# Optimization experiments

Hardware: AMD Instinct MI355X
Metric: run time of the kernel (lower is better)

The kernel has to match this reference:

```python
import jax, jax.numpy as jnp
import numpy as np

B, S, E, H, V, L = 128, 64, 300, 512, 100000, 5


def _linear_params(k, din, dout):
    k1, k2 = jax.random.split(k)
    w = jax.random.normal(k1, (dout, din), jnp.float32) * (1.0 / np.sqrt(din))
    b = jax.random.normal(k2, (dout,), jnp.float32) * 0.01
    return w, b


def setup_inputs() -> dict:
    key = jax.random.key(0)
    ks = jax.random.split(key, 12)
    inp = {}
    inp["x"] = jax.random.randint(ks[0], (B, S), 0, V)              # word ids
    inp["bfs"] = jax.random.randint(ks[1], (B, S), 0, S)            # processing order (node index per step)
    inp["children"] = jax.random.randint(ks[2], (B, S, S), 0, 2).astype(jnp.int32)  # binary child adjacency
    inp["embed"] = jax.random.normal(ks[3], (V, E), jnp.float32) * 0.1
    names = ["ix", "ih", "fx", "fh", "ux", "uh"]
    dims = [(E, H), (H, H), (E, H), (H, H), (E, H), (H, H)]
    for n, (di, do), k in zip(names, dims, ks[4:10]):
        w, b = _linear_params(k, di, do)
        inp["W" + n] = w
        inp["b" + n] = b
    w, b = _linear_params(ks[10], H, L)
    inp["Wout"] = w
    inp["bout"] = b
    return inp


def reference(x, bfs, children, embed,
              Wix, bix, Wih, bih, Wfx, bfx, Wfh, bfh, Wux, bux, Wuh, buh,
              Wout, bout):
    # Child-Sum TreeLSTM processed in BFS order. Dropouts are eval-mode (identity).
    Bb, Ss = x.shape
    Hh = Wih.shape[0]
    xe_all = embed[x]                     # [B,S,E]
    pos = jnp.arange(Ss)

    def step(carry, cur):
        all_C, all_H, _ = carry           # all_C/all_H: [B,S,H]; cur: [B] node index this step
        xe = jnp.take_along_axis(xe_all, cur[:, None, None], axis=1)[:, 0]            # [B,E]
        cmask = jnp.take_along_axis(children, cur[:, None, None], axis=1)[:, 0]       # [B,S]
        cmask = cmask.astype(xe.dtype)
        h_sum = jnp.einsum('bs,bsh->bh', cmask, all_H)                                # sum of child hiddens
        fx_x = xe @ Wfx.T + bfx
        i = jax.nn.sigmoid(xe @ Wix.T + bix + h_sum @ Wih.T + bih)
        # NOTE: faithful to source — the 'o' gate uses fx/fh (ox/oh are dead params)
        o = jax.nn.sigmoid(fx_x + h_sum @ Wfh.T + bfh)
        u = jnp.tanh(xe @ Wux.T + bux + h_sum @ Wuh.T + buh)
        f = jax.nn.sigmoid(all_H @ Wfh.T + bfh + fx_x[:, None, :])                    # [B,S,H] per-child forget
        fc = jnp.einsum('bs,bsh->bh', cmask, f * all_C)                               # masked sum over children
        c = i * u + fc                                                                 # [B,H]
        h = o * jnp.tanh(c)
        onehot = (pos[None, :] == cur[:, None])[:, :, None]                           # [B,S,1]
        all_C = jnp.where(onehot, c[:, None, :], all_C)
        all_H = jnp.where(onehot, h[:, None, :], all_H)
        return (all_C, all_H, h), None

    init = (jnp.zeros((Bb, Ss, Hh), embed.dtype),
            jnp.zeros((Bb, Ss, Hh), embed.dtype),
            jnp.zeros((Bb, Hh), embed.dtype))
    (_, _, h_last), _ = jax.lax.scan(step, init, bfs.T)  # scan over sent_len steps
    return h_last @ Wout.T + bout                        # [B, label_num]
```

## Files before the change

### kernel.cpp

```cpp
#include <hip/hip_runtime.h>
#include <math.h>

#define BB 128
#define SS 64
#define EE 300
#define HH 512
#define LL 5
#define BSH (BB*SS*HH)
#define KP  320
#define NGRP 8
#define BPG  32
#define HSL  16
#define WSROW 520
#define HS_BASE (2*3*16*WSROW)
#define WS_BYTES ((2*3*16*WSROW + 2*16*WSROW)*2)

typedef __attribute__((ext_vector_type(8))) short bf16x8;
typedef __attribute__((ext_vector_type(4))) float f32x4;
typedef __attribute__((ext_vector_type(4))) unsigned int u32x4;

__device__ __forceinline__ float fast_sigmoid(float x) {
    return 1.0f / (1.0f + __expf(-x));
}
__device__ __forceinline__ float fast_tanh(float x) {
    x = fminf(fmaxf(x, -20.0f), 20.0f);
    float e = __expf(2.0f * x);
    return (e - 1.0f) / (e + 1.0f);
}
__device__ __forceinline__ unsigned short f2bf(float f) {
    unsigned int u = __float_as_uint(f);
    u += 0x7fffu + ((u >> 16) & 1u);
    return (unsigned short)(u >> 16);
}
__device__ __forceinline__ float bf2f(unsigned short h) {
    return __uint_as_float((unsigned int)h << 16);
}
__device__ __forceinline__ void split2(float v, unsigned short& hi, unsigned short& lo) {
    hi = f2bf(v);
    lo = f2bf(v - bf2f(hi));
}

#define LDX4V(dst, addr) \
    asm volatile("global_load_dwordx4 %0, %1, off sc0 sc1" \
                 : "=v"(dst) : "v"(addr))

#define STH(addr, val) \
    asm volatile("global_store_short %0, %1, off sc0 sc1" \
                 :: "v"(addr), "v"(val) : "memory")

__global__ __launch_bounds__(256) void prep_kernel(
    const int* __restrict__ bfs, const int* __restrict__ children,
    const float* __restrict__ Wix, const float* __restrict__ Wfx, const float* __restrict__ Wux,
    const float* __restrict__ Wih, const float* __restrict__ Wfh, const float* __restrict__ Wuh,
    unsigned short* __restrict__ Wixh, unsigned short* __restrict__ Wixl,
    unsigned short* __restrict__ Wfxh, unsigned short* __restrict__ Wfxl,
    unsigned short* __restrict__ Wuxh, unsigned short* __restrict__ Wuxl,
    unsigned short* __restrict__ Wihh, unsigned short* __restrict__ Wihl,
    unsigned short* __restrict__ Wfhh, unsigned short* __restrict__ Wfhl,
    unsigned short* __restrict__ Wuhh, unsigned short* __restrict__ Wuhl,
    unsigned char* __restrict__ clist, int* __restrict__ ccnt, int* __restrict__ bars)
{
    const int gid = blockIdx.x * 256 + threadIdx.x;
    const int G = gridDim.x * 256;
    for (int i = gid; i < NGRP * SS; i += G) bars[i] = 0;
    for (int i = gid; i < 3 * HH * KP; i += G) {
        int g = i / (HH * KP), rem = i % (HH * KP), r = rem / KP, k = rem % KP;
        const float* src = (g == 0) ? Wix : (g == 1) ? Wfx : Wux;
        unsigned short* dh = (g == 0) ? Wixh : (g == 1) ? Wfxh : Wuxh;
        unsigned short* dl = (g == 0) ? Wixl : (g == 1) ? Wfxl : Wuxl;
        float v = (k < EE) ? src[(size_t)r * EE + k] : 0.0f;
        unsigned short hi, lo; split2(v, hi, lo);
        dh[r * KP + k] = hi; dl[r * KP + k] = lo;
    }
    for (int i = gid; i < 3 * HH * HH; i += G) {
        int g = i / (HH * HH), idx = i % (HH * HH);
        const float* src = (g == 0) ? Wih : (g == 1) ? Wfh : Wuh;
        unsigned short* dh = (g == 0) ? Wihh : (g == 1) ? Wfhh : Wuhh;
        unsigned short* dl = (g == 0) ? Wihl : (g == 1) ? Wfhl : Wuhl;
        unsigned short hi, lo; split2(src[idx], hi, lo);
        dh[idx] = hi; dl[idx] = lo;
    }
    if (gid < BB * SS) {
        const int b = gid >> 6, t = gid & 63;
        unsigned long long w = 0;
        for (int tp = 0; tp < t; ++tp) w |= 1ull << (bfs[b * SS + tp] & 63);
        const int cur = bfs[b * SS + t];
        const int* crow = children + (size_t)(b * SS + cur) * SS;
        unsigned char* lst = clist + (size_t)gid * SS;
        int cnt = 0;
        for (int s = 0; s < SS; ++s)
            if (crow[s] != 0 && ((w >> s) & 1ull)) lst[cnt++] = (unsigned char)s;
        ccnt[gid] = cnt;
    }
}

__global__ __launch_bounds__(256) void xp_mfma(
    const int* __restrict__ x, const float* __restrict__ embed,
    const unsigned short* __restrict__ Wixh, const unsigned short* __restrict__ Wixl,
    const unsigned short* __restrict__ Wfxh, const unsigned short* __restrict__ Wfxl,
    const unsigned short* __restrict__ Wuxh, const unsigned short* __restrict__ Wuxl,
    const float* __restrict__ bix, const float* __restrict__ bih,
    const float* __restrict__ bfx, const float* __restrict__ bfh,
    const float* __restrict__ bux, const float* __restrict__ buh,
    float* __restrict__ XPp)
{
    const int mb = blockIdx.x;
    const int g  = blockIdx.y;
    const unsigned short* __restrict__ Wbh = (g == 0) ? Wixh : (g == 1) ? Wfxh : Wuxh;
    const unsigned short* __restrict__ Wbl = (g == 0) ? Wixl : (g == 1) ? Wfxl : Wuxl;
    const float* __restrict__ b1 = (g == 0) ? bix : (g == 1) ? bfx : bux;
    const float* __restrict__ b2 = (g == 0) ? bih : (g == 1) ? bfh : buh;

    const int row0 = mb * 16;
    __shared__ unsigned short As[2][16 * 328];
    __shared__ int toks[16];

    const int tid = threadIdx.x;
    if (tid < 16) toks[tid] = x[row0 + tid];
    __syncthreads();

    for (int i = tid; i < 16 * 75; i += 256) {
        int r = i / 75, c = i - r * 75;
        const float4 v = *(const float4*)(embed + (size_t)toks[r] * EE + c * 4);
        ushort4 hv, lv;
        split2(v.x, hv.x, lv.x); split2(v.y, hv.y, lv.y);
        split2(v.z, hv.z, lv.z); split2(v.w, hv.w, lv.w);
        *(ushort4*)&As[0][r * 328 + c * 4] = hv;
        *(ushort4*)&As[1][r * 328 + c * 4] = lv;
    }
    for (int i = tid; i < 16 * 20; i += 256) {
        int r = i / 20, k = EE + (i - r * 20);
        As[0][r * 328 + k] = 0; As[1][r * 328 + k] = 0;
    }
    __syncthreads();

    const int lane = tid & 63, wave = tid >> 6;
    const int quad = lane >> 4, col = lane & 15;
    const int wn = wave * 16;

    for (int nt = 0; nt < 8; ++nt) {
        const int gn = nt * 64 + wn + col;
        const size_t wrow = (size_t)gn * KP;
        f32x4 accA = {0.f, 0.f, 0.f, 0.f}, accB = {0.f, 0.f, 0.f, 0.f};
        #pragma unroll
        for (int kq = 0; kq < 10; ++kq) {
            const int ka = kq * 32 + quad * 8;
            bf16x8 bh = *(const bf16x8*)(Wbh + wrow + ka);
            bf16x8 bl = *(const bf16x8*)(Wbl + wrow + ka);
            bf16x8 ah = *(const bf16x8*)&As[0][col * 328 + ka];
            bf16x8 al = *(const bf16x8*)&As[1][col * 328 + ka];
            accA = __builtin_amdgcn_mfma_f32_16x16x32_bf16(ah, bh, accA, 0, 0, 0);
            accB = __builtin_amdgcn_mfma_f32_16x16x32_bf16(ah, bl, accB, 0, 0, 0);
            accA = __builtin_amdgcn_mfma_f32_16x16x32_bf16(al, bh, accA, 0, 0, 0);
        }
        const f32x4 acc = accA + accB;
        const float bb = b1[gn] + b2[gn];
        #pragma unroll
        for (int reg = 0; reg < 4; ++reg) {
            const int ml = quad * 4 + reg;
            XPp[((size_t)(row0 + ml) * HH + gn) * 4 + g] = acc[reg] + bb;
        }
    }
}

__global__ __launch_bounds__(256, 1) void fused_steps(
    const int* __restrict__ bfs, const unsigned char* __restrict__ clist,
    const int* __restrict__ ccnt, const float* __restrict__ XPp,
    const unsigned short* __restrict__ Wihh, const unsigned short* __restrict__ Wihl,
    const unsigned short* __restrict__ Wfhh, const unsigned short* __restrict__ Wfhl,
    const unsigned short* __restrict__ Wuhh, const unsigned short* __restrict__ Wuhl,
    float* __restrict__ HWC, float* __restrict__ hf32,
    unsigned short* __restrict__ h_hi, unsigned short* __restrict__ h_lo,
    int* __restrict__ bars)
{
    extern __shared__ unsigned short Ws[];
    __shared__ int s_cur[16 * 64];
    __shared__ int s_cnt[16 * 64];
    __shared__ unsigned char s_cl[16 * 64];

    const int g = blockIdx.x & 7;
    const int l = blockIdx.x >> 3;
    const int tid = threadIdx.x;
    const int m0 = g * 16;
    const int n0 = l * HSL;

    const int lane = tid & 63, wave = tid >> 6;
    const int quad = lane >> 4, col = lane & 15;

    const int chain = tid >> 4, hl = tid & 15;
    const int b = m0 + chain;
    const int h = n0 + hl;

    {
        for (int i = tid; i < 6144; i += 256) {
            const int plane = i / 3072, rem = i % 3072;
            const int gt = rem / 1024, rem2 = rem % 1024;
            const int r = rem2 >> 6, c = rem2 & 63;
            const unsigned short* src =
                (plane == 0) ? ((gt == 0) ? Wihh : (gt == 1) ? Wfhh : Wuhh)
                             : ((gt == 0) ? Wihl : (gt == 1) ? Wfhl : Wuhl);
            *(u32x4*)&Ws[((plane * 3 + gt) * 16 + r) * WSROW + c * 8] =
                *(const u32x4*)(src + (size_t)(n0 + r) * HH + c * 8);
        }
        for (int i = tid; i < 16 * 64; i += 256) {
            s_cur[i] = bfs[(m0 + (i >> 6)) * SS + (i & 63)];
            s_cnt[i] = ccnt[(m0 + (i >> 6)) * SS + (i & 63)];
        }
        if (tid < 64) {
            const int ch = tid >> 2, c = tid & 3;
            ((u32x4*)s_cl)[tid] =
                *(const u32x4*)(clist + ((size_t)(m0 + ch) * SS + 0) * SS + c * 16);
        }
    }
    __syncthreads();

    const size_t browf = (size_t)b * (SS * HH * 4);
    float4 xp_c, xp_n;
    {
        const int cur0 = s_cur[(chain << 6) + 0];
        xp_c = *(const float4*)(XPp + browf + (size_t)cur0 * (HH * 4) + h * 4);
    }

    int* gbars = bars + g * SS;

    int st_p[8], st_ch[8], st_o16[8];
    #pragma unroll
    for (int j = 0; j < 8; ++j) {
        const int i = j * 256 + tid;
        st_p[j] = i >> 10; st_ch[j] = (i & 1023) >> 6; st_o16[j] = i & 63;
    }

    for (int t = 0; t < SS; ++t) {
        const int cur = s_cur[(chain << 6) + t];
        const int cnt = s_cnt[(chain << 6) + t];
        const float xpi = xp_c.x, xpf = xp_c.y, xpu = xp_c.z;
        const float* HWb = HWC + browf + h * 4;
        const unsigned char* clp = &s_cl[chain << 6];

        float ai = 0.f, af = 0.f, au = 0.f, fc = 0.f;
        int idx = 0;
        while (idx + 8 <= cnt) {
            const float4 v0 = *(const float4*)(HWb + (size_t)clp[idx + 0] * 2048);
            const float4 v1 = *(const float4*)(HWb + (size_t)clp[idx + 1] * 2048);
            const float4 v2 = *(const float4*)(HWb + (size_t)clp[idx + 2] * 2048);
            const float4 v3 = *(const float4*)(HWb + (size_t)clp[idx + 3] * 2048);
            const float4 v4 = *(const float4*)(HWb + (size_t)clp[idx + 4] * 2048);
            const float4 v5 = *(const float4*)(HWb + (size_t)clp[idx + 5] * 2048);
            const float4 v6 = *(const float4*)(HWb + (size_t)clp[idx + 6] * 2048);
            const float4 v7 = *(const float4*)(HWb + (size_t)clp[idx + 7] * 2048);
            ai += v0.x + v1.x + v2.x + v3.x + v4.x + v5.x + v6.x + v7.x;
            af += v0.y + v1.y + v2.y + v3.y + v4.y + v5.y + v6.y + v7.y;
            au += v0.z + v1.z + v2.z + v3.z + v4.z + v5.z + v6.z + v7.z;
            fc += fast_sigmoid(v0.y + xpf) * v0.w + fast_sigmoid(v1.y + xpf) * v1.w
                + fast_sigmoid(v2.y + xpf) * v2.w + fast_sigmoid(v3.y + xpf) * v3.w
                + fast_sigmoid(v4.y + xpf) * v4.w + fast_sigmoid(v5.y + xpf) * v5.w
                + fast_sigmoid(v6.y + xpf) * v6.w + fast_sigmoid(v7.y + xpf) * v7.w;
            idx += 8;
        }
        while (idx + 4 <= cnt) {
            const float4 v0 = *(const float4*)(HWb + (size_t)clp[idx + 0] * 2048);
            const float4 v1 = *(const float4*)(HWb + (size_t)clp[idx + 1] * 2048);
            const float4 v2 = *(const float4*)(HWb + (size_t)clp[idx + 2] * 2048);
            const float4 v3 = *(const float4*)(HWb + (size_t)clp[idx + 3] * 2048);
            ai += v0.x + v1.x + v2.x + v3.x;
            af += v0.y + v1.y + v2.y + v3.y;
            au += v0.z + v1.z + v2.z + v3.z;
            fc += fast_sigmoid(v0.y + xpf) * v0.w + fast_sigmoid(v1.y + xpf) * v1.w
                + fast_sigmoid(v2.y + xpf) * v2.w + fast_sigmoid(v3.y + xpf) * v3.w;
            idx += 4;
        }
        while (idx < cnt) {
            const float4 v = *(const float4*)(HWb + (size_t)clp[idx] * 2048);
            ai += v.x; af += v.y; au += v.z;
            fc += fast_sigmoid(v.y + xpf) * v.w;
            ++idx;
        }

        const float ig = fast_sigmoid(xpi + ai);
        const float og = fast_sigmoid(xpf + af);
        const float ug = fast_tanh(xpu + au);
        const float c  = ig * ug + fc;
        const float hv = og * fast_tanh(c);

        HWC[browf + (size_t)cur * 2048 + h * 4 + 3] = c;
        if (t == SS - 1) {
            hf32[(size_t)b * HH + h] = hv;
            break;
        }
        {
            unsigned short hh_s, hlo_s; split2(hv, hh_s, hlo_s);
            const unsigned long long ah = (unsigned long long)(h_hi + (size_t)b * HH + h);
            const unsigned long long al = (unsigned long long)(h_lo + (size_t)b * HH + h);
            STH(ah, (unsigned int)hh_s);
            STH(al, (unsigned int)hlo_s);
        }

        __asm__ volatile("s_waitcnt vmcnt(0)" ::: "memory");
        __syncthreads();

        {
            const int curn = s_cur[(chain << 6) + t + 1];
            xp_n = *(const float4*)(XPp + browf + (size_t)curn * (HH * 4) + h * 4);
        }
        if (tid == 0) {
            int* cntp = gbars + t;
            __hip_atomic_fetch_add(cntp, 1, __ATOMIC_RELAXED, __HIP_MEMORY_SCOPE_AGENT);
            while (__hip_atomic_load(cntp, __ATOMIC_RELAXED, __HIP_MEMORY_SCOPE_AGENT) < BPG)
                __builtin_amdgcn_s_sleep(1);
        }
        __syncthreads();

        if (wave == 3 && lane < 64) {
            const int ch = lane >> 2, cc = lane & 3;
            ((u32x4*)s_cl)[lane] =
                *(const u32x4*)(clist + ((size_t)(m0 + ch) * SS + (t + 1)) * SS + cc * 16);
        }
        {
            u32x4 st0, st1, st2, st3, st4, st5, st6, st7;
            const unsigned long long a0 = (unsigned long long)((st_p[0] ? h_lo : h_hi) + (size_t)(m0 + st_ch[0]) * HH + st_o16[0] * 8);
            const unsigned long long a1 = (unsigned long long)((st_p[1] ? h_lo : h_hi) + (size_t)(m0 + st_ch[1]) * HH + st_o16[1] * 8);
            const unsigned long long a2 = (unsigned long long)((st_p[2] ? h_lo : h_hi) + (size_t)(m0 + st_ch[2]) * HH + st_o16[2] * 8);
            const unsigned long long a3 = (unsigned long long)((st_p[3] ? h_lo : h_hi) + (size_t)(m0 + st_ch[3]) * HH + st_o16[3] * 8);
            const unsigned long long a4 = (unsigned long long)((st_p[4] ? h_lo : h_hi) + (size_t)(m0 + st_ch[4]) * HH + st_o16[4] * 8);
            const unsigned long long a5 = (unsigned long long)((st_p[5] ? h_lo : h_hi) + (size_t)(m0 + st_ch[5]) * HH + st_o16[5] * 8);
            const unsigned long long a6 = (unsigned long long)((st_p[6] ? h_lo : h_hi) + (size_t)(m0 + st_ch[6]) * HH + st_o16[6] * 8);
            const unsigned long long a7 = (unsigned long long)((st_p[7] ? h_lo : h_hi) + (size_t)(m0 + st_ch[7]) * HH + st_o16[7] * 8);
            LDX4V(st0, a0); LDX4V(st1, a1); LDX4V(st2, a2); LDX4V(st3, a3);
            LDX4V(st4, a4); LDX4V(st5, a5); LDX4V(st6, a6); LDX4V(st7, a7);
            asm volatile("s_waitcnt vmcnt(0)" ::: "memory");
            __builtin_amdgcn_sched_barrier(0);
            *(u32x4*)&Ws[HS_BASE + (st_p[0] * 16 + st_ch[0]) * WSROW + st_o16[0] * 8] = st0;
            *(u32x4*)&Ws[HS_BASE + (st_p[1] * 16 + st_ch[1]) * WSROW + st_o16[1] * 8] = st1;
            *(u32x4*)&Ws[HS_BASE + (st_p[2] * 16 + st_ch[2]) * WSROW + st_o16[2] * 8] = st2;
            *(u32x4*)&Ws[HS_BASE + (st_p[3] * 16 + st_ch[3]) * WSROW + st_o16[3] * 8] = st3;
            *(u32x4*)&Ws[HS_BASE + (st_p[4] * 16 + st_ch[4]) * WSROW + st_o16[4] * 8] = st4;
            *(u32x4*)&Ws[HS_BASE + (st_p[5] * 16 + st_ch[5]) * WSROW + st_o16[5] * 8] = st5;
            *(u32x4*)&Ws[HS_BASE + (st_p[6] * 16 + st_ch[6]) * WSROW + st_o16[6] * 8] = st6;
            *(u32x4*)&Ws[HS_BASE + (st_p[7] * 16 + st_ch[7]) * WSROW + st_o16[7] * 8] = st7;
        }
        __syncthreads();

        if (wave < 3) {
            f32x4 accA = {0.f, 0.f, 0.f, 0.f}, accB = {0.f, 0.f, 0.f, 0.f};
            const int ha0 = HS_BASE + (0 * 16 + col) * WSROW;
            const int ha1 = HS_BASE + (1 * 16 + col) * WSROW;
            #pragma unroll
            for (int kq = 0; kq < 16; ++kq) {
                const int ka = kq * 32 + quad * 8;
                bf16x8 ahv = *(const bf16x8*)&Ws[ha0 + ka];
                bf16x8 alv = *(const bf16x8*)&Ws[ha1 + ka];
                bf16x8 bh = *(const bf16x8*)&Ws[((0 * 3 + wave) * 16 + col) * WSROW + ka];
                bf16x8 bl = *(const bf16x8*)&Ws[((1 * 3 + wave) * 16 + col) * WSROW + ka];
                accA = __builtin_amdgcn_mfma_f32_16x16x32_bf16(ahv, bh, accA, 0, 0, 0);
                accB = __builtin_amdgcn_mfma_f32_16x16x32_bf16(ahv, bl, accB, 0, 0, 0);
                accA = __builtin_amdgcn_mfma_f32_16x16x32_bf16(alv, bh, accA, 0, 0, 0);
            }
            const f32x4 acc = accA + accB;
            #pragma unroll
            for (int reg = 0; reg < 4; ++reg) {
                const int m = quad * 4 + reg;
                const int curm = s_cur[(m << 6) + t];
                HWC[(size_t)(m0 + m) * (SS * HH * 4) + (size_t)curm * 2048
                    + (n0 + col) * 4 + wave] = acc[reg];
            }
        }
        __threadfence_block();
        __syncthreads();
        xp_c = xp_n;
    }
}

__global__ __launch_bounds__(64) void out_kernel(
    const float* __restrict__ hcur,
    const float* __restrict__ Wout, const float* __restrict__ bout,
    float* __restrict__ out)
{
    const int b = blockIdx.x;
    const int lane = threadIdx.x;
    float acc[LL];
    #pragma unroll
    for (int l = 0; l < LL; ++l) acc[l] = 0.0f;
    for (int h = lane; h < HH; h += 64) {
        const float hv = hcur[(size_t)b * HH + h];
        #pragma unroll
        for (int l = 0; l < LL; ++l) acc[l] += hv * Wout[l * HH + h];
    }
    #pragma unroll
    for (int off = 32; off > 0; off >>= 1) {
        #pragma unroll
        for (int l = 0; l < LL; ++l) acc[l] += __shfl_down(acc[l], off);
    }
    if (lane == 0) {
        #pragma unroll
        for (int l = 0; l < LL; ++l) out[b * LL + l] = acc[l] + bout[l];
    }
}

extern "C" void kernel_launch(void* const* d_in, const int* in_sizes, int n_in,
                              void* d_out, int out_size, void* d_ws, size_t ws_size,
                              hipStream_t stream)
{
    (void)in_sizes; (void)n_in; (void)out_size; (void)ws_size;
    const int*   x        = (const int*)d_in[0];
    const int*   bfs      = (const int*)d_in[1];
    const int*   children = (const int*)d_in[2];
    const float* embed    = (const float*)d_in[3];
    const float* Wix = (const float*)d_in[4];
    const float* bix = (const float*)d_in[5];
    const float* Wih = (const float*)d_in[6];
    const float* bih = (const float*)d_in[7];
    const float* Wfx = (const float*)d_in[8];
    const float* bfx = (const float*)d_in[9];
    const float* Wfh = (const float*)d_in[10];
    const float* bfh = (const float*)d_in[11];
    const float* Wux = (const float*)d_in[12];
    const float* bux = (const float*)d_in[13];
    const float* Wuh = (const float*)d_in[14];
    const float* buh = (const float*)d_in[15];
    const float* Wout = (const float*)d_in[16];
    const float* bout = (const float*)d_in[17];
    float* out = (float*)d_out;

    char* p = (char*)d_ws;
    float* XPp = (float*)p;            p += (size_t)BSH * 4 * 4;
    float* HWC = (float*)p;            p += (size_t)BSH * 4 * 4;
    float* hf32 = (float*)p;           p += (size_t)BB * HH * 4;
    unsigned short* h_hi = (unsigned short*)p; p += (size_t)BB * HH * 2;
    unsigned short* h_lo = (unsigned short*)p; p += (size_t)BB * HH * 2;
    unsigned short* Wixh = (unsigned short*)p; p += (size_t)HH * KP * 2;
    unsigned short* Wixl = (unsigned short*)p; p += (size_t)HH * KP * 2;
    unsigned short* Wfxh = (unsigned short*)p; p += (size_t)HH * KP * 2;
    unsigned short* Wfxl = (unsigned short*)p; p += (size_t)HH * KP * 2;
    unsigned short* Wuxh = (unsigned short*)p; p += (size_t)HH * KP * 2;
    unsigned short* Wuxl = (unsigned short*)p; p += (size_t)HH * KP * 2;
    unsigned short* Wihh = (unsigned short*)p; p += (size_t)HH * HH * 2;
    unsigned short* Wihl = (unsigned short*)p; p += (size_t)HH * HH * 2;
    unsigned short* Wfhh = (unsigned short*)p; p += (size_t)HH * HH * 2;
    unsigned short* Wfhl = (unsigned short*)p; p += (size_t)HH * HH * 2;
    unsigned short* Wuhh = (unsigned short*)p; p += (size_t)HH * HH * 2;
    unsigned short* Wuhl = (unsigned short*)p; p += (size_t)HH * HH * 2;
    unsigned char* clist = (unsigned char*)p;  p += (size_t)BB * SS * SS;
    int* ccnt = (int*)p;               p += (size_t)BB * SS * 4;
    int* bars = (int*)p;               p += (size_t)NGRP * SS * 4;

    (void)hipFuncSetAttribute((const void*)fused_steps,
                              hipFuncAttributeMaxDynamicSharedMemorySize,
                              WS_BYTES);

    prep_kernel<<<dim3(256), 256, 0, stream>>>(
        bfs, children, Wix, Wfx, Wux, Wih, Wfh, Wuh,
        Wixh, Wixl, Wfxh, Wfxl, Wuxh, Wuxl,
        Wihh, Wihl, Wfhh, Wfhl, Wuhh, Wuhl, clist, ccnt, bars);

    xp_mfma<<<dim3(512, 3), 256, 0, stream>>>(
        x, embed, Wixh, Wixl, Wfxh, Wfxl, Wuxh, Wuxl,
        bix, bih, bfx, bfh, bux, buh, XPp);

    {
        void* args[] = {
            (void*)&bfs, (void*)&clist, (void*)&ccnt, (void*)&XPp,
            (void*)&Wihh, (void*)&Wihl, (void*)&Wfhh, (void*)&Wfhl,
            (void*)&Wuhh, (void*)&Wuhl,
            (void*)&HWC, (void*)&hf32, (void*)&h_hi, (void*)&h_lo, (void*)&bars
        };
        hipLaunchCooperativeKernel((void*)fused_steps, dim3(NGRP * BPG), dim3(256),
                                   args, WS_BYTES, stream);
    }

    out_kernel<<<dim3(BB), 64, 0, stream>>>(hf32, Wout, bout, out);
}
```

Before: 827.9 us.

## Replace per-step group barrier with step-tagged hidden-state flags in double buffer

Each hidden-state value is now stored as a 64-bit word that packs the bf16 hi/lo halves with a step tag, in a double-buffered array. Consumers poll their gathered loads until every tag matches the current step. This removes the atomic counter barrier, the vmcnt drain and one __syncthreads per step, so data arrival itself signals readiness. In exchange it doubles the size of the exchanged data, adds spin-polling reloads and relies on the 64-bit stores being observed atomically.

```diff
diff --git a/kernel.cpp b/kernel.cpp
--- a/kernel.cpp
+++ b/kernel.cpp
@@ -40,13 +40,9 @@
     lo = f2bf(v - bf2f(hi));
 }
 
-#define LDX4V(dst, addr) \
-    asm volatile("global_load_dwordx4 %0, %1, off sc0 sc1" \
-                 : "=v"(dst) : "v"(addr))
-
-#define STH(addr, val) \
-    asm volatile("global_store_short %0, %1, off sc0 sc1" \
-                 :: "v"(addr), "v"(val) : "memory")
+#define LDT(dst, OFF) \
+    asm volatile("global_load_dwordx4 %0, %1, off offset:" #OFF " sc0 sc1" \
+                 : "=v"(dst) : "v"(hb))
 
 __global__ __launch_bounds__(256) void prep_kernel(
     const int* __restrict__ bfs, const int* __restrict__ children,
@@ -58,11 +54,17 @@
     unsigned short* __restrict__ Wihh, unsigned short* __restrict__ Wihl,
     unsigned short* __restrict__ Wfhh, unsigned short* __restrict__ Wfhl,
     unsigned short* __restrict__ Wuhh, unsigned short* __restrict__ Wuhl,
-    unsigned char* __restrict__ clist, int* __restrict__ ccnt, int* __restrict__ bars)
+    unsigned char* __restrict__ clist, int* __restrict__ ccnt,
+    unsigned long long* __restrict__ h_tag)
 {
     const int gid = blockIdx.x * 256 + threadIdx.x;
     const int G = gridDim.x * 256;
-    for (int i = gid; i < NGRP * SS; i += G) bars[i] = 0;
+    for (int i = gid; i < 2 * BB * HH; i += G) {
+        const unsigned long long a = (unsigned long long)(h_tag + i);
+        const unsigned long long z = 0ull;
+        asm volatile("global_store_dwordx2 %0, %1, off sc0 sc1"
+                     :: "v"(a), "v"(z) : "memory");
+    }
     for (int i = gid; i < 3 * HH * KP; i += G) {
         int g = i / (HH * KP), rem = i % (HH * KP), r = rem / KP, k = rem % KP;
         const float* src = (g == 0) ? Wix : (g == 1) ? Wfx : Wux;
@@ -170,8 +172,7 @@
     const unsigned short* __restrict__ Wfhh, const unsigned short* __restrict__ Wfhl,
     const unsigned short* __restrict__ Wuhh, const unsigned short* __restrict__ Wuhl,
     float* __restrict__ HWC, float* __restrict__ hf32,
-    unsigned short* __restrict__ h_hi, unsigned short* __restrict__ h_lo,
-    int* __restrict__ bars)
+    unsigned long long* __restrict__ h_tag)
 {
     extern __shared__ unsigned short Ws[];
     __shared__ int s_cur[16 * 64];
@@ -221,14 +222,8 @@
         xp_c = *(const float4*)(XPp + browf + (size_t)cur0 * (HH * 4) + h * 4);
     }
 
-    int* gbars = bars + g * SS;
-
-    int st_p[8], st_ch[8], st_o16[8];
-    #pragma unroll
-    for (int j = 0; j < 8; ++j) {
-        const int i = j * 256 + tid;
-        st_p[j] = i >> 10; st_ch[j] = (i & 1023) >> 6; st_o16[j] = i & 63;
-    }
+    const int st_ch = tid >> 4;
+    const int st_h0 = (tid & 15) * 32;
 
     for (int t = 0; t < SS; ++t) {
         const int cur = s_cur[(chain << 6) + t];
@@ -289,25 +284,19 @@
         }
         {
             unsigned short hh_s, hlo_s; split2(hv, hh_s, hlo_s);
-            const unsigned long long ah = (unsigned long long)(h_hi + (size_t)b * HH + h);
-            const unsigned long long al = (unsigned long long)(h_lo + (size_t)b * HH + h);
-            STH(ah, (unsigned int)hh_s);
-            STH(al, (unsigned int)hlo_s);
-        }
-
-        __asm__ volatile("s_waitcnt vmcnt(0)" ::: "memory");
-        __syncthreads();
-
+            const unsigned long long payload =
+                ((unsigned long long)(unsigned int)(t + 1) << 32)
+                | ((unsigned int)hh_s << 16) | (unsigned int)hlo_s;
+            const unsigned long long addr = (unsigned long long)(h_tag
+                + (size_t)(t & 1) * (BB * HH) + (size_t)b * HH + h);
+            asm volatile("global_store_dwordx2 %0, %1, off sc0 sc1"
+                         :: "v"(addr), "v"(payload) : "memory");
+        }
         {
             const int curn = s_cur[(chain << 6) + t + 1];
             xp_n = *(const float4*)(XPp + browf + (size_t)curn * (HH * 4) + h * 4);
         }
-        if (tid == 0) {
-            int* cntp = gbars + t;
-            __hip_atomic_fetch_add(cntp, 1, __ATOMIC_RELAXED, __HIP_MEMORY_SCOPE_AGENT);
-            while (__hip_atomic_load(cntp, __ATOMIC_RELAXED, __HIP_MEMORY_SCOPE_AGENT) < BPG)
-                __builtin_amdgcn_s_sleep(1);
-        }
+
         __syncthreads();
 
         if (wave == 3 && lane < 64) {
@@ -316,27 +305,60 @@
                 *(const u32x4*)(clist + ((size_t)(m0 + ch) * SS + (t + 1)) * SS + cc * 16);
         }
         {
-            u32x4 st0, st1, st2, st3, st4, st5, st6, st7;
-            const unsigned long long a0 = (unsigned long long)((st_p[0] ? h_lo : h_hi) + (size_t)(m0 + st_ch[0]) * HH + st_o16[0] * 8);
-            const unsigned long long a1 = (unsigned long long)((st_p[1] ? h_lo : h_hi) + (size_t)(m0 + st_ch[1]) * HH + st_o16[1] * 8);
-            const unsigned long long a2 = (unsigned long long)((st_p[2] ? h_lo : h_hi) + (size_t)(m0 + st_ch[2]) * HH + st_o16[2] * 8);
-            const unsigned long long a3 = (unsigned long long)((st_p[3] ? h_lo : h_hi) + (size_t)(m0 + st_ch[3]) * HH + st_o16[3] * 8);
-            const unsigned long long a4 = (unsigned long long)((st_p[4] ? h_lo : h_hi) + (size_t)(m0 + st_ch[4]) * HH + st_o16[4] * 8);
-            const unsigned long long a5 = (unsigned long long)((st_p[5] ? h_lo : h_hi) + (size_t)(m0 + st_ch[5]) * HH + st_o16[5] * 8);
-            const unsigned long long a6 = (unsigned long long)((st_p[6] ? h_lo : h_hi) + (size_t)(m0 + st_ch[6]) * HH + st_o16[6] * 8);
-            const unsigned long long a7 = (unsigned long long)((st_p[7] ? h_lo : h_hi) + (size_t)(m0 + st_ch[7]) * HH + st_o16[7] * 8);
-            LDX4V(st0, a0); LDX4V(st1, a1); LDX4V(st2, a2); LDX4V(st3, a3);
-            LDX4V(st4, a4); LDX4V(st5, a5); LDX4V(st6, a6); LDX4V(st7, a7);
-            asm volatile("s_waitcnt vmcnt(0)" ::: "memory");
-            __builtin_amdgcn_sched_barrier(0);
-            *(u32x4*)&Ws[HS_BASE + (st_p[0] * 16 + st_ch[0]) * WSROW + st_o16[0] * 8] = st0;
-            *(u32x4*)&Ws[HS_BASE + (st_p[1] * 16 + st_ch[1]) * WSROW + st_o16[1] * 8] = st1;
-            *(u32x4*)&Ws[HS_BASE + (st_p[2] * 16 + st_ch[2]) * WSROW + st_o16[2] * 8] = st2;
-            *(u32x4*)&Ws[HS_BASE + (st_p[3] * 16 + st_ch[3]) * WSROW + st_o16[3] * 8] = st3;
-            *(u32x4*)&Ws[HS_BASE + (st_p[4] * 16 + st_ch[4]) * WSROW + st_o16[4] * 8] = st4;
-            *(u32x4*)&Ws[HS_BASE + (st_p[5] * 16 + st_ch[5]) * WSROW + st_o16[5] * 8] = st5;
-            *(u32x4*)&Ws[HS_BASE + (st_p[6] * 16 + st_ch[6]) * WSROW + st_o16[6] * 8] = st6;
-            *(u32x4*)&Ws[HS_BASE + (st_p[7] * 16 + st_ch[7]) * WSROW + st_o16[7] * 8] = st7;
+            const unsigned long long hb = (unsigned long long)(h_tag
+                + (size_t)(t & 1) * (BB * HH) + (size_t)(m0 + st_ch) * HH + st_h0);
+            const unsigned int want = (unsigned int)(t + 1);
+            u32x4 r0, r1, r2, r3, r4, r5, r6, r7, r8, r9, r10, r11, r12, r13, r14, r15;
+            for (;;) {
+                LDT(r0,   0); LDT(r1,  16); LDT(r2,  32); LDT(r3,  48);
+                LDT(r4,  64); LDT(r5,  80); LDT(r6,  96); LDT(r7, 112);
+                LDT(r8, 128); LDT(r9, 144); LDT(r10,160); LDT(r11,176);
+                LDT(r12,192); LDT(r13,208); LDT(r14,224); LDT(r15,240);
+                asm volatile("s_waitcnt vmcnt(0)" ::: "memory");
+                __builtin_amdgcn_sched_barrier(0);
+                unsigned int ok =
+                      (unsigned int)(r0.y == want) & (unsigned int)(r0.w == want)
+                    & (unsigned int)(r1.y == want) & (unsigned int)(r1.w == want)
+                    & (unsigned int)(r2.y == want) & (unsigned int)(r2.w == want)
+                    & (unsigned int)(r3.y == want) & (unsigned int)(r3.w == want)
+                    & (unsigned int)(r4.y == want) & (unsigned int)(r4.w == want)
+                    & (unsigned int)(r5.y == want) & (unsigned int)(r5.w == want)
+                    & (unsigned int)(r6.y == want) & (unsigned int)(r6.w == want)
+                    & (unsigned int)(r7.y == want) & (unsigned int)(r7.w == want)
+                    & (unsigned int)(r8.y == want) & (unsigned int)(r8.w == want)
+                    & (unsigned int)(r9.y == want) & (unsigned int)(r9.w == want)
+                    & (unsigned int)(r10.y == want) & (unsigned int)(r10.w == want)
+                    & (unsigned int)(r11.y == want) & (unsigned int)(r11.w == want)
+                    & (unsigned int)(r12.y == want) & (unsigned int)(r12.w == want)
+                    & (unsigned int)(r13.y == want) & (unsigned int)(r13.w == want)
+                    & (unsigned int)(r14.y == want) & (unsigned int)(r14.w == want)
+                    & (unsigned int)(r15.y == want) & (unsigned int)(r15.w == want);
+                if (__all((int)ok)) break;
+            }
+            #define HIW(r) (((r).x >> 16) | ((r).z & 0xffff0000u))
+            #define LOW(r) (((r).x & 0xffffu) | ((r).z << 16))
+            {
+                u32x4 hv0 = {HIW(r0), HIW(r1), HIW(r2), HIW(r3)};
+                u32x4 hv1 = {HIW(r4), HIW(r5), HIW(r6), HIW(r7)};
+                u32x4 hv2 = {HIW(r8), HIW(r9), HIW(r10), HIW(r11)};
+                u32x4 hv3 = {HIW(r12), HIW(r13), HIW(r14), HIW(r15)};
+                u32x4 lv0 = {LOW(r0), LOW(r1), LOW(r2), LOW(r3)};
+                u32x4 lv1 = {LOW(r4), LOW(r5), LOW(r6), LOW(r7)};
+                u32x4 lv2 = {LOW(r8), LOW(r9), LOW(r10), LOW(r11)};
+                u32x4 lv3 = {LOW(r12), LOW(r13), LOW(r14), LOW(r15)};
+                const int hbase = HS_BASE + st_ch * WSROW + st_h0;
+                *(u32x4*)&Ws[hbase +  0] = hv0;
+                *(u32x4*)&Ws[hbase +  8] = hv1;
+                *(u32x4*)&Ws[hbase + 16] = hv2;
+                *(u32x4*)&Ws[hbase + 24] = hv3;
+                const int lbase = HS_BASE + (16 + st_ch) * WSROW + st_h0;
+                *(u32x4*)&Ws[lbase +  0] = lv0;
+                *(u32x4*)&Ws[lbase +  8] = lv1;
+                *(u32x4*)&Ws[lbase + 16] = lv2;
+                *(u32x4*)&Ws[lbase + 24] = lv3;
+            }
+            #undef HIW
+            #undef LOW
         }
         __syncthreads();
 
@@ -425,8 +447,8 @@
     float* XPp = (float*)p;            p += (size_t)BSH * 4 * 4;
     float* HWC = (float*)p;            p += (size_t)BSH * 4 * 4;
     float* hf32 = (float*)p;           p += (size_t)BB * HH * 4;
-    unsigned short* h_hi = (unsigned short*)p; p += (size_t)BB * HH * 2;
-    unsigned short* h_lo = (unsigned short*)p; p += (size_t)BB * HH * 2;
+    unsigned long long* h_tag = (unsigned long long*)p;
+    p += (size_t)2 * BB * HH * 8;
     unsigned short* Wixh = (unsigned short*)p; p += (size_t)HH * KP * 2;
     unsigned short* Wixl = (unsigned short*)p; p += (size_t)HH * KP * 2;
     unsigned short* Wfxh = (unsigned short*)p; p += (size_t)HH * KP * 2;
@@ -441,7 +463,6 @@
     unsigned short* Wuhl = (unsigned short*)p; p += (size_t)HH * HH * 2;
     unsigned char* clist = (unsigned char*)p;  p += (size_t)BB * SS * SS;
     int* ccnt = (int*)p;               p += (size_t)BB * SS * 4;
-    int* bars = (int*)p;               p += (size_t)NGRP * SS * 4;
 
     (void)hipFuncSetAttribute((const void*)fused_steps,
                               hipFuncAttributeMaxDynamicSharedMemorySize,
@@ -450,7 +471,7 @@
     prep_kernel<<<dim3(256), 256, 0, stream>>>(
         bfs, children, Wix, Wfx, Wux, Wih, Wfh, Wuh,
         Wixh, Wixl, Wfxh, Wfxl, Wuxh, Wuxl,
-        Wihh, Wihl, Wfhh, Wfhl, Wuhh, Wuhl, clist, ccnt, bars);
+        Wihh, Wihl, Wfhh, Wfhl, Wuhh, Wuhl, clist, ccnt, h_tag);
 
     xp_mfma<<<dim3(512, 3), 256, 0, stream>>>(
         x, embed, Wixh, Wixl, Wfxh, Wfxl, Wuxh, Wuxl,
@@ -461,7 +482,7 @@
             (void*)&bfs, (void*)&clist, (void*)&ccnt, (void*)&XPp,
             (void*)&Wihh, (void*)&Wihl, (void*)&Wfhh, (void*)&Wfhl,
             (void*)&Wuhh, (void*)&Wuhl,
-            (void*)&HWC, (void*)&hf32, (void*)&h_hi, (void*)&h_lo, (void*)&bars
+            (void*)&HWC, (void*)&hf32, (void*)&h_tag
         };
         hipLaunchCooperativeKernel((void*)fused_steps, dim3(NGRP * BPG), dim3(256),
                                    args, WS_BYTES, stream);
```

After: 1.058 ms. 27.8% more time.
